# Optimization experiments

Measured on AMD Instinct MI355X. Metric: run time of the kernel, lower is better.

The kernel has to match this reference:

```python
import jax, jax.numpy as jnp
import numpy as np

NUM_ENT = 10000
NUM_REL = 50
HID = 64
N_TRIP = 500000


def _ramp_layer(emb_ent, emb_rel, W_res, W_me, W_mr, W_pr, h, r, t):
    num_ent, num_rel = emb_ent.shape[0], emb_rel.shape[0]
    d_out = W_me.shape[0] // num_rel
    # relation-specific projections: (num_ent, num_rel, d_out), (num_rel, num_rel, d_out)
    proj_ent = (emb_ent @ W_me.T).reshape(num_ent, num_rel, d_out)
    proj_rel = (emb_rel @ W_mr.T).reshape(num_rel, num_rel, d_out)
    diag_rel = proj_rel[jnp.arange(num_rel), jnp.arange(num_rel)]  # (num_rel, d_out)
    # gather per-triplet messages: proj_ent[h, r] + proj_rel[r, r]
    msg = proj_ent[h, r] + diag_rel[r]  # (T, d_out)
    # aggr_method == 'sum' -> div_coeff = 1
    upd = (emb_ent @ W_res.T).at[t].add(msg)  # scatter-add into tails
    return jax.nn.leaky_relu(upd, negative_slope=0.01), emb_rel @ W_pr.T


def setup_inputs() -> dict:
    key = jax.random.key(0)
    ks = jax.random.split(key, 11)
    gain = float(np.sqrt(2.0))  # relu gain

    def xavier(k, shape):
        fan_out, fan_in = shape
        std = gain * np.sqrt(2.0 / (fan_in + fan_out))
        return (jax.random.normal(k, shape, dtype=jnp.float32) * std)

    def msg_init(k, shape, d_in, d_out):
        std = gain * np.sqrt(2.0 / (d_in + d_out))
        return (jax.random.normal(k, shape, dtype=jnp.float32) * std)

    inp = {
        # layer 0: dim_in_ent=NUM_ENT, dim_in_rel=NUM_REL, dim_out=HID
        "Wres0": xavier(ks[0], (HID, NUM_ENT)),
        "Wme0": msg_init(ks[1], (NUM_REL * HID, NUM_ENT), NUM_ENT, HID),
        "Wmr0": msg_init(ks[2], (NUM_REL * HID, NUM_REL), NUM_REL, HID),
        "Wpr0": xavier(ks[3], (HID, NUM_REL)),
        # layer 1: dim_in_ent=HID, dim_in_rel=HID
        "Wres1": xavier(ks[4], (HID, HID)),
        "Wme1": msg_init(ks[5], (NUM_REL * HID, HID), HID, HID),
        "Wmr1": msg_init(ks[6], (NUM_REL * HID, HID), HID, HID),
        "Wpr1": xavier(ks[7], (HID, HID)),
        "h": jax.random.randint(ks[8], (N_TRIP,), 0, NUM_ENT),
        "r": jax.random.randint(ks[9], (N_TRIP,), 0, NUM_REL),
        "t": jax.random.randint(ks[10], (N_TRIP,), 0, NUM_ENT),
    }
    return inp


def reference(Wres0, Wme0, Wmr0, Wpr0, Wres1, Wme1, Wmr1, Wpr1, h, r, t):
    emb_ent = jnp.eye(NUM_ENT, dtype=jnp.float32)
    emb_rel = jnp.eye(NUM_REL, dtype=jnp.float32)
    emb_ent, emb_rel = _ramp_layer(emb_ent, emb_rel, Wres0, Wme0, Wmr0, Wpr0, h, r, t)
    emb_ent, emb_rel = _ramp_layer(emb_ent, emb_rel, Wres1, Wme1, Wmr1, Wpr1, h, r, t)
    return (emb_ent, emb_rel)
```

## Files before the change

kernel.cpp:

```cpp
#include <hip/hip_runtime.h>

#define NUM_ENT 10000
#define NUM_REL 50
#define HID 64
#define NTRIP 500000
#define NSLOT 51
#define SSTR (NUM_ENT * HID)
#define ETILE 128
#define NETILE 79
#define TRB (NSLOT * NETILE)

typedef __attribute__((ext_vector_type(8))) short short8;
typedef __attribute__((ext_vector_type(4))) float f32x4;

static __device__ __forceinline__ unsigned short f2bf(float x) {
    unsigned u = __float_as_uint(x);
    return (unsigned short)((u + 0x7FFFu + ((u >> 16) & 1u)) >> 16);
}
static __device__ __forceinline__ float bf2f(unsigned short b) {
    return __uint_as_float((unsigned)b << 16);
}
static __device__ __forceinline__ short8 ld8(const unsigned short* p) {
    return *(const short8*)p;
}


__global__ __launch_bounds__(256) void k_prep(const float* __restrict__ Wmr0,
                                              const float* __restrict__ Wpr0,
                                              const float* __restrict__ Wmr1,
                                              const float* __restrict__ Wpr1,
                                              const float* __restrict__ Wme1,
                                              const float* __restrict__ Wres1,
                                              int* __restrict__ bins,
                                              float* __restrict__ diag0,
                                              float* __restrict__ diag1,
                                              float* __restrict__ outrel,
                                              unsigned short* __restrict__ Wb) {
    int bid = blockIdx.x, tid = threadIdx.x;
    if (bid < 40) {
        int i = bid * 256 + tid;
        if (i < NUM_ENT) bins[i] = 0;
        return;
    }
    bid -= 40;
    if (bid < 13) {
        int i = bid * 256 + tid;
        if (i < NSLOT * HID)
            diag0[i] = (i < NUM_REL * HID) ? Wmr0[(size_t)i * NUM_REL + (i >> 6)] : 0.f;
        return;
    }
    bid -= 13;
    if (bid < 13) {
        __shared__ float wp[4][64];
        int sub = tid >> 6, d = tid & 63;
        int rr = bid * 4 + sub;
        wp[sub][d] = (rr < NUM_REL) ? Wpr0[d * NUM_REL + rr] : 0.f;
        __syncthreads();
        if (rr < NUM_REL) {
            float s1 = 0.f, s2 = 0.f;
            const float* wmr = Wmr1 + (size_t)(rr * HID + d) * HID;
            const float* wpr = Wpr1 + d * HID;
            for (int k = 0; k < HID; k++) {
                s1 += wp[sub][k] * wmr[k];
                s2 += wp[sub][k] * wpr[k];
            }
            diag1[rr * HID + d] = s1;
            outrel[rr * HID + d] = s2;
        }
        return;
    }
    bid -= 13;
    if (bid < 816) {
        int i = bid * 256 + tid;
        if (i < NSLOT * HID * HID)
            Wb[i] = f2bf(i < NUM_REL * HID * HID ? Wme1[i]
                                                 : Wres1[i - NUM_REL * HID * HID]);
        return;
    }
    if (tid < HID) diag1[NUM_REL * HID + tid] = 0.f;
}


__global__ __launch_bounds__(256) void k_rank(const int* __restrict__ t,
                                              int* __restrict__ bins,
                                              int* __restrict__ rank) {
    int i = blockIdx.x * 256 + threadIdx.x;
    if (i < NTRIP) rank[i] = atomicAdd(&bins[t[i]], 1);
}

__global__ __launch_bounds__(1024) void k_scan(const int* __restrict__ bins,
                                               int* __restrict__ toff, int nbins) {
    __shared__ int wsum[16];
    int tid = threadIdx.x, lane = tid & 63, w = tid >> 6;
    int running = 0;
    for (int base = 0; base < nbins; base += 1024) {
        int i = base + tid;
        int s = (i < nbins) ? bins[i] : 0;
        int v = s;
        for (int off = 1; off < 64; off <<= 1) {
            int u = __shfl_up(v, off);
            if (lane >= off) v += u;
        }
        if (lane == 63) wsum[w] = v;
        __syncthreads();
        int woff = 0, tot = 0;
#pragma unroll
        for (int k = 0; k < 16; ++k) {
            int x = wsum[k];
            woff += (k < w) ? x : 0;
            tot += x;
        }
        int excl = running + woff + (v - s);
        if (i < nbins) toff[i] = excl;
        running += tot;
        __syncthreads();
    }
    if (tid == 0) toff[nbins] = running;
}


__global__ __launch_bounds__(256) void k_build(const float* __restrict__ Wme0,
                                               const float* __restrict__ Wres0,
                                               const float* __restrict__ diag0,
                                               unsigned short* __restrict__ P,
                                               const int* __restrict__ h,
                                               const int* __restrict__ r,
                                               const int* __restrict__ t,
                                               const int* __restrict__ rank,
                                               const int* __restrict__ toff,
                                               unsigned* __restrict__ bucket2) {
    __shared__ __align__(16) unsigned utile[ETILE][32];
    __shared__ float dg[64];
    int tid = threadIdx.x;

    if (blockIdx.x >= TRB) {
        int i = ((int)blockIdx.x - TRB) * 256 + tid;
        if (i < NTRIP)
            bucket2[toff[t[i]] + rank[i]] =
                (unsigned)r[i] * (unsigned)SSTR + (unsigned)h[i] * 64u;
        return;
    }

    int slot = blockIdx.x / NETILE;
    int ey = blockIdx.x - slot * NETILE;
    int e0 = ey * ETILE;
    const float* Wbase = (slot < NUM_REL)
        ? Wme0 + (size_t)(slot * HID) * NUM_ENT + e0
        : Wres0 + e0;
    unsigned short* Pslot = P + (size_t)slot * SSTR;

    if (e0 + ETILE <= NUM_ENT) {
        int dp = tid >> 5;
        int kk = tid & 31;
        int x4 = kk * 4;
        int wf1 = kk & 7;
        int wf2 = kk >> 3;
        const float* p0 = Wbase + (size_t)(dp * 2 + 0) * NUM_ENT + x4;
        const float* p1 = Wbase + (size_t)(dp * 2 + 1) * NUM_ENT + x4;
        float4 vA0 = *(const float4*)(p0);
        float4 vB0 = *(const float4*)(p1);
        float4 vA1 = *(const float4*)(p0 + 16 * NUM_ENT);
        float4 vB1 = *(const float4*)(p1 + 16 * NUM_ENT);
        float4 vA2 = *(const float4*)(p0 + 32 * NUM_ENT);
        float4 vB2 = *(const float4*)(p1 + 32 * NUM_ENT);
        float4 vA3 = *(const float4*)(p0 + 48 * NUM_ENT);
        float4 vB3 = *(const float4*)(p1 + 48 * NUM_ENT);

        if (tid < 64) dg[tid] = diag0[slot * HID + tid];
        __syncthreads();

#define PACK_IT(IT, VA, VB)                                                     \
        {                                                                       \
            int d = IT * 16 + dp * 2;                                           \
            int d2 = IT * 8 + dp;                                               \
            float dgA = dg[d], dgB = dg[d + 1];                                 \
            const float* a = (const float*)&VA;                                 \
            const float* b = (const float*)&VB;                                 \
            int col = (((d2 >> 2) ^ wf1) << 2) | ((d2 & 3) ^ wf2);              \
            utile[x4 + 0][col] = (unsigned)f2bf(a[0] + dgA) |                   \
                                 ((unsigned)f2bf(b[0] + dgB) << 16);            \
            utile[x4 + 1][col] = (unsigned)f2bf(a[1] + dgA) |                   \
                                 ((unsigned)f2bf(b[1] + dgB) << 16);            \
            utile[x4 + 2][col] = (unsigned)f2bf(a[2] + dgA) |                   \
                                 ((unsigned)f2bf(b[2] + dgB) << 16);            \
            utile[x4 + 3][col] = (unsigned)f2bf(a[3] + dgA) |                   \
                                 ((unsigned)f2bf(b[3] + dgB) << 16);            \
        }
        PACK_IT(0, vA0, vB0)
        PACK_IT(1, vA1, vB1)
        PACK_IT(2, vA2, vB2)
        PACK_IT(3, vA3, vB3)
#undef PACK_IT
        __syncthreads();
#pragma unroll
        for (int it = 0; it < 4; ++it) {
            int idx = tid + it * 256;
            int ee = idx >> 3;
            int q = idx & 7;
            int f1 = (ee >> 2) & 7;
            int f2 = (ee >> 5) & 3;
            uint4 u = *(const uint4*)&utile[ee][(q ^ f1) << 2];
            unsigned ua = u.x, ub = u.y, uc = u.z, ud = u.w;
            if (f2 & 1) { unsigned s0 = ua; ua = ub; ub = s0;
                          unsigned s1 = uc; uc = ud; ud = s1; }
            if (f2 & 2) { unsigned s0 = ua; ua = uc; uc = s0;
                          unsigned s1 = ub; ub = ud; ud = s1; }
            uint4 o = make_uint4(ua, ub, uc, ud);
            *(uint4*)&Pslot[(size_t)(e0 + ee) * 64 + q * 8] = o;
        }
    } else {
        if (tid < 64) dg[tid] = diag0[slot * HID + tid];
        __syncthreads();
        int rem = NUM_ENT - e0;
        for (int i = tid; i < rem * 64; i += 256) {
            int ee = i % rem;
            int dd = i / rem;
            float v = Wbase[(size_t)dd * NUM_ENT + ee] + dg[dd];
            Pslot[(size_t)(e0 + ee) * 64 + dd] = f2bf(v);
        }
    }
}


__global__ __launch_bounds__(256) void k_gemmB(const unsigned short* __restrict__ Abf,
                                               const unsigned short* __restrict__ Wb,
                                               const float* __restrict__ diag1,
                                               unsigned short* __restrict__ B,
                                               int percut) {
    int e0 = blockIdx.x * 64;
    int rl0 = blockIdx.y * percut;
    int rl1 = rl0 + percut;
    if (rl1 > NSLOT) rl1 = NSLOT;
    int w = (int)threadIdx.x >> 6;
    int lane = (int)threadIdx.x & 63;
    int lrow = lane & 15;
    int hi = lane >> 4;
    int lk8 = hi * 8;
    int row = e0 + w * 16 + lrow;
    int rowc = row < NUM_ENT ? row : NUM_ENT - 1;
    short8 a0 = ld8(Abf + (size_t)rowc * HID + lk8);
    short8 a1 = ld8(Abf + (size_t)rowc * HID + 32 + lk8);

    for (int rl = rl0; rl < rl1; ++rl) {
        const unsigned short* wb = Wb + (size_t)rl * 4096;
        f32x4 acc[4] = {};
#pragma unroll
        for (int tt = 0; tt < 4; ++tt) {
            const unsigned short* wd = wb + (tt * 16 + lrow) * 64;
            short8 b0 = ld8(wd + lk8);
            short8 b1 = ld8(wd + 32 + lk8);
            acc[tt] = __builtin_amdgcn_mfma_f32_16x16x32_bf16(a0, b0, acc[tt], 0, 0, 0);
            acc[tt] = __builtin_amdgcn_mfma_f32_16x16x32_bf16(a1, b1, acc[tt], 0, 0, 0);
        }
        unsigned short* Bslot = B + (size_t)rl * SSTR;
#pragma unroll
        for (int tt = 0; tt < 4; ++tt) {
            float dgv = diag1[rl * HID + tt * 16 + lrow];
#pragma unroll
            for (int q = 0; q < 4; ++q) {
                int eo = e0 + w * 16 + hi * 4 + q;
                if (eo < NUM_ENT)
                    Bslot[(size_t)eo * 64 + tt * 16 + lrow] = f2bf(acc[tt][q] + dgv);
            }
        }
    }
}


__global__ __launch_bounds__(256) void k_scatter(const unsigned short* __restrict__ table,
                                                 const int* __restrict__ toff,
                                                 const unsigned* __restrict__ bucket2,
                                                 unsigned short* __restrict__ Abf,
                                                 float* __restrict__ outF,
                                                 int writeBf) {
    int e = __builtin_amdgcn_readfirstlane(blockIdx.x * 4 + (threadIdx.x >> 6));
    if (e >= NUM_ENT) return;
    int lane = threadIdx.x & 63;
    int oct = lane >> 3;
    int sl = lane & 7;
    int j0 = toff[e], j1 = toff[e + 1];
    float acc[8] = {};
    float acc2[8] = {};
    int jj = j0;
    for (; jj + 16 <= j1; jj += 16) {
        unsigned o0 = bucket2[jj + oct];
        unsigned o1 = bucket2[jj + 8 + oct];
        short8 v0 = ld8(table + o0 + sl * 8);
        short8 v1 = ld8(table + o1 + sl * 8);
#pragma unroll
        for (int k = 0; k < 8; ++k) {
            acc[k]  += bf2f(((const unsigned short*)&v0)[k]);
            acc2[k] += bf2f(((const unsigned short*)&v1)[k]);
        }
    }
    if (jj + 8 <= j1) {
        unsigned o = bucket2[jj + oct];
        short8 v = ld8(table + o + sl * 8);
#pragma unroll
        for (int k = 0; k < 8; ++k) acc[k] += bf2f(((const unsigned short*)&v)[k]);
        jj += 8;
    }
    if (oct < j1 - jj) {
        unsigned o = bucket2[jj + oct];
        short8 v = ld8(table + o + sl * 8);
#pragma unroll
        for (int k = 0; k < 8; ++k) acc2[k] += bf2f(((const unsigned short*)&v)[k]);
    }
#pragma unroll
    for (int k = 0; k < 8; ++k) {
        acc[k] += acc2[k];
        acc[k] += __shfl_xor(acc[k], 8);
        acc[k] += __shfl_xor(acc[k], 16);
        acc[k] += __shfl_xor(acc[k], 32);
    }
    if (oct == 0) {
        short8 base = ld8(table + (size_t)(NSLOT - 1) * SSTR + (size_t)e * HID + sl * 8);
        float v[8];
#pragma unroll
        for (int k = 0; k < 8; ++k) {
            float x = acc[k] + bf2f(((const unsigned short*)&base)[k]);
            v[k] = (x >= 0.f) ? x : 0.01f * x;
        }
        if (writeBf) {
            unsigned short pk[8];
#pragma unroll
            for (int k = 0; k < 8; ++k) pk[k] = f2bf(v[k]);
            *(short8*)&Abf[(size_t)e * HID + sl * 8] = *(const short8*)pk;
        } else {
            *(float4*)&outF[(size_t)e * HID + sl * 8] = make_float4(v[0], v[1], v[2], v[3]);
            *(float4*)&outF[(size_t)e * HID + sl * 8 + 4] = make_float4(v[4], v[5], v[6], v[7]);
        }
    }
}


__global__ void k_rel(const float* __restrict__ Wpr0, const float* __restrict__ Wmr1,
                      const float* __restrict__ Wpr1, float* __restrict__ diag1,
                      float* __restrict__ outrel) {
    __shared__ float wp[HID];
    int rr = blockIdx.x, d = threadIdx.x;
    wp[d] = Wpr0[d * NUM_REL + rr];
    __syncthreads();
    float s1 = 0.0f, s2 = 0.0f;
    const float* wmr = Wmr1 + (size_t)(rr * HID + d) * HID;
    const float* wpr = Wpr1 + d * HID;
    for (int k = 0; k < HID; k++) { s1 += wp[k] * wmr[k]; s2 += wp[k] * wpr[k]; }
    diag1[rr * HID + d] = s1;
    outrel[rr * HID + d] = s2;
}

__global__ void k_init_u0(const float* __restrict__ Wres0, float* __restrict__ U0) {
    __shared__ float tile[64][65];
    int e0 = blockIdx.x * 64;
    for (int i = threadIdx.x; i < 64 * 64; i += 256) {
        int dd = i >> 6, xx = i & 63;
        if (e0 + xx < NUM_ENT) tile[xx][dd] = Wres0[dd * NUM_ENT + e0 + xx];
    }
    __syncthreads();
    for (int i = threadIdx.x; i < 64 * 64; i += 256) {
        int ee = i >> 6, dd = i & 63;
        if (e0 + ee < NUM_ENT) U0[(e0 + ee) * HID + dd] = tile[ee][dd];
    }
}

__global__ void k_hist(const int* __restrict__ r, int* __restrict__ hist) {
    __shared__ int lh[NUM_REL];
    int tid = threadIdx.x;
    if (tid < NUM_REL) lh[tid] = 0;
    __syncthreads();
    int i = blockIdx.x * blockDim.x + tid;
    if (i < NTRIP) atomicAdd(&lh[r[i]], 1);
    __syncthreads();
    if (tid < NUM_REL && lh[tid] > 0) atomicAdd(&hist[tid], lh[tid]);
}

__global__ void k_scan_small(const int* __restrict__ hist, int* __restrict__ off,
                             int* __restrict__ cur) {
    if (threadIdx.x == 0 && blockIdx.x == 0) {
        int s = 0;
        for (int i = 0; i < NUM_REL; i++) { off[i] = s; cur[i] = s; s += hist[i]; }
        off[NUM_REL] = s;
    }
}

__global__ void k_bucket(const int* __restrict__ h, const int* __restrict__ r,
                         const int* __restrict__ t, int* __restrict__ cur,
                         int2* __restrict__ bucket) {
    __shared__ int lcnt[NUM_REL];
    __shared__ int lbase[NUM_REL];
    int tid = threadIdx.x;
    if (tid < NUM_REL) lcnt[tid] = 0;
    __syncthreads();
    int i = blockIdx.x * blockDim.x + tid;
    int rr = -1, lpos = 0;
    if (i < NTRIP) { rr = r[i]; lpos = atomicAdd(&lcnt[rr], 1); }
    __syncthreads();
    if (tid < NUM_REL && lcnt[tid] > 0) lbase[tid] = atomicAdd(&cur[tid], lcnt[tid]);
    __syncthreads();
    if (i < NTRIP) bucket[lbase[rr] + lpos] = make_int2(h[i], t[i]);
}

__global__ void k_l0(const float* __restrict__ Wme0, const float* __restrict__ Wmr0,
                     const int* __restrict__ off, const int2* __restrict__ bucket,
                     float* __restrict__ U0) {
    __shared__ float row[NUM_ENT];
    int rr = blockIdx.x >> 6;
    int d  = blockIdx.x & 63;
    const float4* src4 = (const float4*)(Wme0 + (size_t)(rr * HID + d) * NUM_ENT);
    float4* row4 = (float4*)row;
    for (int i = threadIdx.x; i < NUM_ENT / 4; i += blockDim.x) row4[i] = src4[i];
    __syncthreads();
    float wd0 = Wmr0[(size_t)(rr * HID + d) * NUM_REL + rr];
    int b0 = off[rr], b1 = off[rr + 1];
    for (int i = b0 + threadIdx.x; i < b1; i += blockDim.x) {
        int2 ht = bucket[i];
        atomicAdd(&U0[(size_t)ht.y * HID + d], row[ht.x] + wd0);
    }
}

__global__ void k_lrelu(float* __restrict__ x, int n) {
    int i = blockIdx.x * blockDim.x + threadIdx.x;
    if (i < n) { float v = x[i]; x[i] = v >= 0.0f ? v : 0.01f * v; }
}

__global__ void k_init_u1(const float* __restrict__ A, const float* __restrict__ Wres1,
                          float* __restrict__ out) {
    __shared__ float W[HID][HID + 1];
    int tid = threadIdx.x;
    for (int i = tid; i < HID * HID; i += 256) W[i >> 6][i & 63] = Wres1[i];
    __syncthreads();
    int g = blockIdx.x * 256 + tid;
    int e = g >> 6, d = g & 63;
    if (e >= NUM_ENT) return;
    const float4* arow = (const float4*)(A + (size_t)e * HID);
    float acc = 0.0f;
#pragma unroll
    for (int k4 = 0; k4 < 16; k4++) {
        float4 a = arow[k4];
        acc = fmaf(a.x, W[d][k4 * 4 + 0], acc);
        acc = fmaf(a.y, W[d][k4 * 4 + 1], acc);
        acc = fmaf(a.z, W[d][k4 * 4 + 2], acc);
        acc = fmaf(a.w, W[d][k4 * 4 + 3], acc);
    }
    out[g] = acc;
}

#define L1_CHUNKS 16
__global__ void k_l1(const float* __restrict__ A, const float* __restrict__ Wme1,
                     const int* __restrict__ off, const int2* __restrict__ bucket,
                     const float* __restrict__ diag1, float* __restrict__ out) {
    int rr = blockIdx.x / L1_CHUNKS;
    int chunk = blockIdx.x % L1_CHUNKS;
    int b0 = off[rr], b1 = off[rr + 1];
    for (int i = b0 + chunk * 256 + (int)threadIdx.x; i < b1; i += L1_CHUNKS * 256) {
        int2 ht = bucket[i];
        const float4* arow = (const float4*)(A + (size_t)ht.x * HID);
        float4 a[16];
#pragma unroll
        for (int j = 0; j < 16; j++) a[j] = arow[j];
        float* op = out + (size_t)ht.y * HID;
#pragma unroll 4
        for (int d = 0; d < HID; d++) {
            const float4* m4 = (const float4*)(Wme1 + (size_t)(rr * HID + d) * HID);
            float acc = diag1[rr * HID + d];
#pragma unroll
            for (int k = 0; k < 16; k++) {
                float4 m = m4[k];
                acc = fmaf(a[k].x, m.x, acc);
                acc = fmaf(a[k].y, m.y, acc);
                acc = fmaf(a[k].z, m.z, acc);
                acc = fmaf(a[k].w, m.w, acc);
            }
            atomicAdd(op + d, acc);
        }
    }
}


static inline size_t align_up(size_t x, size_t a) { return (x + a - 1) & ~(a - 1); }

extern "C" void kernel_launch(void* const* d_in, const int* in_sizes, int n_in,
                              void* d_out, int out_size, void* d_ws, size_t ws_size,
                              hipStream_t stream) {
    const float* Wres0 = (const float*)d_in[0];
    const float* Wme0  = (const float*)d_in[1];
    const float* Wmr0  = (const float*)d_in[2];
    const float* Wpr0  = (const float*)d_in[3];
    const float* Wres1 = (const float*)d_in[4];
    const float* Wme1  = (const float*)d_in[5];
    const float* Wmr1  = (const float*)d_in[6];
    const float* Wpr1  = (const float*)d_in[7];
    const int* h = (const int*)d_in[8];
    const int* r = (const int*)d_in[9];
    const int* t = (const int*)d_in[10];
    float* out = (float*)d_out;

    char* ws = (char*)d_ws;
    const int nbt = (NTRIP + 255) / 256;
    const int net = (NUM_ENT + 63) / 64;

    size_t p = 0;
    size_t oTab  = p; p += align_up((size_t)NSLOT * SSTR * 2, 256);
    size_t oB2   = p; p += align_up((size_t)NTRIP * 4, 256);
    size_t oToff = p; p += align_up(((size_t)NUM_ENT + 1) * 4, 256);
    size_t oBins = p; p += align_up((size_t)NUM_ENT * 4, 256);
    size_t oRank = p; p += align_up((size_t)NTRIP * 4, 256);
    size_t oAbf  = p; p += align_up((size_t)NUM_ENT * HID * 2, 256);
    size_t oD0   = p; p += align_up((size_t)NSLOT * HID * 4, 256);
    size_t oD1   = p; p += align_up((size_t)NSLOT * HID * 4, 256);
    size_t oWb   = p; p += align_up((size_t)NSLOT * HID * HID * 2, 256);
    size_t need = p;

    if (need <= ws_size) {
        unsigned short* Tab = (unsigned short*)(ws + oTab);
        unsigned* bucket2   = (unsigned*)(ws + oB2);
        int*      toff      = (int*)(ws + oToff);
        int*      bins      = (int*)(ws + oBins);
        int*      rank      = (int*)(ws + oRank);
        unsigned short* Abf = (unsigned short*)(ws + oAbf);
        float*    diag0     = (float*)(ws + oD0);
        float*    diag1     = (float*)(ws + oD1);
        unsigned short* Wb  = (unsigned short*)(ws + oWb);
        const int nsplit = 6;
        const int percut = (NSLOT + nsplit - 1) / nsplit;

        k_prep<<<883, 256, 0, stream>>>(Wmr0, Wpr0, Wmr1, Wpr1, Wme1, Wres1,
                                        bins, diag0, diag1, out + NUM_ENT * HID, Wb);
        k_rank<<<nbt, 256, 0, stream>>>(t, bins, rank);
        k_scan<<<1, 1024, 0, stream>>>(bins, toff, NUM_ENT);
        k_build<<<TRB + nbt, 256, 0, stream>>>(Wme0, Wres0, diag0, Tab,
                                               h, r, t, rank, toff, bucket2);
        k_scatter<<<(NUM_ENT + 3) / 4, 256, 0, stream>>>(
            Tab, toff, bucket2, Abf, out, 1);
        k_gemmB<<<dim3(net, nsplit), 256, 0, stream>>>(Abf, Wb, diag1, Tab, percut);
        k_scatter<<<(NUM_ENT + 3) / 4, 256, 0, stream>>>(
            Tab, toff, bucket2, Abf, out, 0);
        return;
    }

    {
        int2*  bucket = (int2*)ws;
        float* U0     = (float*)(ws + 4000000);
        float* diag1  = (float*)(ws + 6560000);
        int*   hist   = (int*)(ws + 6572800);
        int*   off    = (int*)(ws + 6573056);
        int*   cur    = (int*)(ws + 6573312);

        hipMemsetAsync(hist, 0, NUM_REL * sizeof(int), stream);
        k_hist<<<nbt, 256, 0, stream>>>(r, hist);
        k_scan_small<<<1, 64, 0, stream>>>(hist, off, cur);
        k_bucket<<<nbt, 256, 0, stream>>>(h, r, t, cur, bucket);

        k_init_u0<<<net, 256, 0, stream>>>(Wres0, U0);
        k_l0<<<NUM_REL * HID, 256, 0, stream>>>(Wme0, Wmr0, off, bucket, U0);
        k_lrelu<<<(NUM_ENT * HID + 255) / 256, 256, 0, stream>>>(U0, NUM_ENT * HID);

        k_rel<<<NUM_REL, HID, 0, stream>>>(Wpr0, Wmr1, Wpr1, diag1, out + NUM_ENT * HID);
        k_init_u1<<<(NUM_ENT * HID) / 256, 256, 0, stream>>>(U0, Wres1, out);
        k_l1<<<NUM_REL * L1_CHUNKS, 256, 0, stream>>>(U0, Wme1, off, bucket, diag1, out);
        k_lrelu<<<(NUM_ENT * HID + 255) / 256, 256, 0, stream>>>(out, NUM_ENT * HID);
    }
}
```

Before: 169.9 us.

## Split layer-0 table build into a bf16 convert pass and a transpose pass

The fused k_build kernel that read fp32 Wme0/Wres0, added the diagonal, converted to bf16 and transposed through LDS is split in two. A first pass does a coalesced row-wise conversion to a bf16 staging buffer and runs alongside the rank atomics. A second pass transposes the bf16 data into the slot table. The aim is to move the fp32 read out of the transpose kernel and overlap it with the rank pass, at the cost of an extra ~65MB bf16 write and read plus more workspace.

```diff
diff --git a/kernel.cpp b/kernel.cpp
--- a/kernel.cpp
+++ b/kernel.cpp
@@ -9,6 +9,9 @@
 #define ETILE 128
 #define NETILE 79
 #define TRB (NSLOT * NETILE)
+#define NROW (NSLOT * HID)
+#define NCHK 5
+#define NCONV (NROW * NCHK)
 
 typedef __attribute__((ext_vector_type(8))) short short8;
 typedef __attribute__((ext_vector_type(4))) float f32x4;
@@ -81,12 +84,37 @@
 }
 
 
-__global__ __launch_bounds__(256) void k_rank(const int* __restrict__ t,
-                                              int* __restrict__ bins,
-                                              int* __restrict__ rank) {
-    int i = blockIdx.x * 256 + threadIdx.x;
-    if (i < NTRIP) rank[i] = atomicAdd(&bins[t[i]], 1);
-}
+__global__ __launch_bounds__(256) void k_pass1(const float* __restrict__ Wme0,
+                                               const float* __restrict__ Wres0,
+                                               const float* __restrict__ diag0,
+                                               unsigned short* __restrict__ Wbf,
+                                               const int* __restrict__ t,
+                                               int* __restrict__ bins,
+                                               int* __restrict__ rank) {
+    int tid = threadIdx.x;
+    if (blockIdx.x >= NCONV) {
+        int i = ((int)blockIdx.x - NCONV) * 256 + tid;
+        if (i < NTRIP) rank[i] = atomicAdd(&bins[t[i]], 1);
+        return;
+    }
+    int row = blockIdx.x / NCHK;
+    int chunk = blockIdx.x - row * NCHK;
+    int e0 = chunk * 2048 + tid * 8;
+    if (tid * 8 >= 2048 || e0 >= NUM_ENT) return;
+    float dgv = diag0[row];
+    const float* src = (row < NUM_REL * HID)
+        ? Wme0 + (size_t)row * NUM_ENT
+        : Wres0 + (size_t)(row - NUM_REL * HID) * NUM_ENT;
+    float4 a = *(const float4*)(src + e0);
+    float4 b = *(const float4*)(src + e0 + 4);
+    unsigned short pk[8];
+    pk[0] = f2bf(a.x + dgv); pk[1] = f2bf(a.y + dgv);
+    pk[2] = f2bf(a.z + dgv); pk[3] = f2bf(a.w + dgv);
+    pk[4] = f2bf(b.x + dgv); pk[5] = f2bf(b.y + dgv);
+    pk[6] = f2bf(b.z + dgv); pk[7] = f2bf(b.w + dgv);
+    *(short8*)&Wbf[(size_t)row * NUM_ENT + e0] = *(const short8*)pk;
+}
+
 
 __global__ __launch_bounds__(1024) void k_scan(const int* __restrict__ bins,
                                                int* __restrict__ toff, int nbins) {
@@ -119,9 +147,7 @@
 }
 
 
-__global__ __launch_bounds__(256) void k_build(const float* __restrict__ Wme0,
-                                               const float* __restrict__ Wres0,
-                                               const float* __restrict__ diag0,
+__global__ __launch_bounds__(256) void k_pass2(const unsigned short* __restrict__ Wbf,
                                                unsigned short* __restrict__ P,
                                                const int* __restrict__ h,
                                                const int* __restrict__ r,
@@ -130,7 +156,6 @@
                                                const int* __restrict__ toff,
                                                unsigned* __restrict__ bucket2) {
     __shared__ __align__(16) unsigned utile[ETILE][32];
-    __shared__ float dg[64];
     int tid = threadIdx.x;
 
     if (blockIdx.x >= TRB) {
@@ -144,53 +169,28 @@
     int slot = blockIdx.x / NETILE;
     int ey = blockIdx.x - slot * NETILE;
     int e0 = ey * ETILE;
-    const float* Wbase = (slot < NUM_REL)
-        ? Wme0 + (size_t)(slot * HID) * NUM_ENT + e0
-        : Wres0 + e0;
+    const unsigned short* Wslot = Wbf + (size_t)slot * HID * NUM_ENT;
     unsigned short* Pslot = P + (size_t)slot * SSTR;
 
     if (e0 + ETILE <= NUM_ENT) {
-        int dp = tid >> 5;
-        int kk = tid & 31;
-        int x4 = kk * 4;
-        int wf1 = kk & 7;
-        int wf2 = kk >> 3;
-        const float* p0 = Wbase + (size_t)(dp * 2 + 0) * NUM_ENT + x4;
-        const float* p1 = Wbase + (size_t)(dp * 2 + 1) * NUM_ENT + x4;
-        float4 vA0 = *(const float4*)(p0);
-        float4 vB0 = *(const float4*)(p1);
-        float4 vA1 = *(const float4*)(p0 + 16 * NUM_ENT);
-        float4 vB1 = *(const float4*)(p1 + 16 * NUM_ENT);
-        float4 vA2 = *(const float4*)(p0 + 32 * NUM_ENT);
-        float4 vB2 = *(const float4*)(p1 + 32 * NUM_ENT);
-        float4 vA3 = *(const float4*)(p0 + 48 * NUM_ENT);
-        float4 vB3 = *(const float4*)(p1 + 48 * NUM_ENT);
-
-        if (tid < 64) dg[tid] = diag0[slot * HID + tid];
-        __syncthreads();
-
-#define PACK_IT(IT, VA, VB)                                                     \
-        {                                                                       \
-            int d = IT * 16 + dp * 2;                                           \
-            int d2 = IT * 8 + dp;                                               \
-            float dgA = dg[d], dgB = dg[d + 1];                                 \
-            const float* a = (const float*)&VA;                                 \
-            const float* b = (const float*)&VB;                                 \
-            int col = (((d2 >> 2) ^ wf1) << 2) | ((d2 & 3) ^ wf2);              \
-            utile[x4 + 0][col] = (unsigned)f2bf(a[0] + dgA) |                   \
-                                 ((unsigned)f2bf(b[0] + dgB) << 16);            \
-            utile[x4 + 1][col] = (unsigned)f2bf(a[1] + dgA) |                   \
-                                 ((unsigned)f2bf(b[1] + dgB) << 16);            \
-            utile[x4 + 2][col] = (unsigned)f2bf(a[2] + dgA) |                   \
-                                 ((unsigned)f2bf(b[2] + dgB) << 16);            \
-            utile[x4 + 3][col] = (unsigned)f2bf(a[3] + dgA) |                   \
-                                 ((unsigned)f2bf(b[3] + dgB) << 16);            \
-        }
-        PACK_IT(0, vA0, vB0)
-        PACK_IT(1, vA1, vB1)
-        PACK_IT(2, vA2, vB2)
-        PACK_IT(3, vA3, vB3)
-#undef PACK_IT
+        int rp = tid & 31;
+        int egA = tid >> 5;
+#pragma unroll
+        for (int half = 0; half < 2; ++half) {
+            int eg = egA + half * 8;
+            const unsigned short* rp0 = Wslot + (size_t)(2 * rp) * NUM_ENT + e0 + eg * 8;
+            short8 a = ld8(rp0);
+            short8 b = ld8(rp0 + NUM_ENT);
+            int f2 = eg >> 2;
+#pragma unroll
+            for (int j = 0; j < 8; ++j) {
+                int e = eg * 8 + j;
+                int f1 = (e >> 2) & 7;
+                int col = (((rp >> 2) ^ f1) << 2) | ((rp & 3) ^ f2);
+                utile[e][col] = (unsigned)(unsigned short)a[j] |
+                                ((unsigned)(unsigned short)b[j] << 16);
+            }
+        }
         __syncthreads();
 #pragma unroll
         for (int it = 0; it < 4; ++it) {
@@ -209,14 +209,11 @@
             *(uint4*)&Pslot[(size_t)(e0 + ee) * 64 + q * 8] = o;
         }
     } else {
-        if (tid < 64) dg[tid] = diag0[slot * HID + tid];
-        __syncthreads();
         int rem = NUM_ENT - e0;
         for (int i = tid; i < rem * 64; i += 256) {
             int ee = i % rem;
             int dd = i / rem;
-            float v = Wbase[(size_t)dd * NUM_ENT + ee] + dg[dd];
-            Pslot[(size_t)(e0 + ee) * 64 + dd] = f2bf(v);
+            Pslot[(size_t)(e0 + ee) * 64 + dd] = Wslot[(size_t)dd * NUM_ENT + e0 + ee];
         }
     }
 }
@@ -501,6 +498,7 @@
 
     size_t p = 0;
     size_t oTab  = p; p += align_up((size_t)NSLOT * SSTR * 2, 256);
+    size_t oWbf  = p; p += align_up((size_t)NROW * NUM_ENT * 2, 256);
     size_t oB2   = p; p += align_up((size_t)NTRIP * 4, 256);
     size_t oToff = p; p += align_up(((size_t)NUM_ENT + 1) * 4, 256);
     size_t oBins = p; p += align_up((size_t)NUM_ENT * 4, 256);
@@ -513,6 +511,7 @@
 
     if (need <= ws_size) {
         unsigned short* Tab = (unsigned short*)(ws + oTab);
+        unsigned short* Wbf = (unsigned short*)(ws + oWbf);
         unsigned* bucket2   = (unsigned*)(ws + oB2);
         int*      toff      = (int*)(ws + oToff);
         int*      bins      = (int*)(ws + oBins);
@@ -526,10 +525,10 @@
 
         k_prep<<<883, 256, 0, stream>>>(Wmr0, Wpr0, Wmr1, Wpr1, Wme1, Wres1,
                                         bins, diag0, diag1, out + NUM_ENT * HID, Wb);
-        k_rank<<<nbt, 256, 0, stream>>>(t, bins, rank);
+        k_pass1<<<NCONV + nbt, 256, 0, stream>>>(Wme0, Wres0, diag0, Wbf,
+                                                 t, bins, rank);
         k_scan<<<1, 1024, 0, stream>>>(bins, toff, NUM_ENT);
-        k_build<<<TRB + nbt, 256, 0, stream>>>(Wme0, Wres0, diag0, Tab,
-                                               h, r, t, rank, toff, bucket2);
+        k_pass2<<<TRB + nbt, 256, 0, stream>>>(Wbf, Tab, h, r, t, rank, toff, bucket2);
         k_scatter<<<(NUM_ENT + 3) / 4, 256, 0, stream>>>(
             Tab, toff, bucket2, Abf, out, 1);
         k_gemmB<<<dim3(net, nsplit), 256, 0, stream>>>(Abf, Wb, diag1, Tab, percut);
```

After: 192.1 us. +13.1%, slower.
